# Kernel tuning notes

Measured on AMD Instinct MI355X. Metric: run time of the kernel, lower is better.

The kernel has to match this reference:

```python
import jax, jax.numpy as jnp
import numpy as np

C_M = 256
C_Z = 128
L = 1024


def setup_inputs() -> dict:
    key = jax.random.key(0)
    ks = jax.random.split(key, 8)
    sequence = jax.random.randint(ks[0], (L,), 0, 21)
    residue_index = jnp.arange(L, dtype=jnp.int64) if jax.config.jax_enable_x64 else jnp.arange(L, dtype=jnp.int32)
    # Linear params (torch Linear: y = x @ W.T + b); store as [in, out] for einsum
    W_msa = jax.random.normal(ks[1], (21, C_M), dtype=jnp.float32) * 0.02
    b_msa = jnp.zeros((C_M,), dtype=jnp.float32)
    W_left = jax.random.normal(ks[2], (21, C_Z), dtype=jnp.float32) * 0.02
    b_left = jnp.zeros((C_Z,), dtype=jnp.float32)
    W_right = jax.random.normal(ks[3], (21, C_Z), dtype=jnp.float32) * 0.02
    b_right = jnp.zeros((C_Z,), dtype=jnp.float32)
    relpos_emb = jax.random.normal(ks[4], (65, C_Z), dtype=jnp.float32) * 0.02
    return {
        "sequence": sequence,
        "residue_index": residue_index,
        "W_msa": W_msa, "b_msa": b_msa,
        "W_left": W_left, "b_left": b_left,
        "W_right": W_right, "b_right": b_right,
        "relpos_emb": relpos_emb,
    }


def reference(sequence, residue_index, W_msa, b_msa, W_left, b_left, W_right, b_right, relpos_emb):
    seq = jnp.clip(sequence, 0, 20)
    # one-hot + Linear == row gather of W plus bias; use one_hot matmul to match math exactly
    one_hot = jax.nn.one_hot(seq, 21, dtype=W_msa.dtype)  # [L, 21]
    msa = (one_hot @ W_msa + b_msa)[None]                  # [1, L, c_m]
    left = one_hot @ W_left + b_left                       # [L, c_z]
    right = one_hot @ W_right + b_right                    # [L, c_z]
    d = jnp.clip(residue_index[:, None] - residue_index[None, :] + 32, 0, 64)  # [L, L]
    pair = left[:, None, :] + right[None, :, :] + relpos_emb[d]                # [L, L, c_z]
    return msa, pair
```

## Files before the change

### kernel.cpp

```cpp
#include <hip/hip_runtime.h>

#define L_SEQ 1024
#define CM    256
#define CZ    128
#define NAA   21
#define CHUNK 512
#define NGRP  (CHUNK / 8)

__global__ __launch_bounds__(256, 4) void InputEmbedding_kernel(
    const int*   __restrict__ seq,
    const int*   __restrict__ ri,
    const float* __restrict__ Wm,  const float* __restrict__ bm,
    const float* __restrict__ Wl,  const float* __restrict__ bl,
    const float* __restrict__ Wr,  const float* __restrict__ br,
    const float* __restrict__ rel,
    float* __restrict__ out_msa,
    float* __restrict__ out_pair)
{
    __shared__ float comb   [NAA * CZ];
    __shared__ float comb_lo[NAA * CZ];
    __shared__ float comb_hi[NAA * CZ];
    __shared__ unsigned int sd[CHUNK];

    const int tid = threadIdx.x;
    const int bx  = blockIdx.x;
    const int i   = bx >> 1;
    const int j0  = (bx & 1) * CHUNK;

    int s_i = seq[i];
    s_i = s_i < 0 ? 0 : (s_i > 20 ? 20 : s_i);
    const int rii = ri[i];

    for (int jj = tid; jj < CHUNK; jj += 256) {
        const int j = j0 + jj;
        int sj = seq[j];
        sj = sj < 0 ? 0 : (sj > 20 ? 20 : sj);
        int d = rii - ri[j] + 32;
        d = d < 0 ? 0 : (d > 64 ? 64 : d);
        sd[jj] = (unsigned)(sj * 512) | ((unsigned)(d * 512) << 16);
    }
    for (int idx = tid; idx < NAA * CZ; idx += 256) {
        const int c = idx & (CZ - 1);
        const float cmb = (Wl[s_i * CZ + c] + bl[c]) + (Wr[idx] + br[c]);
        comb[idx]    = cmb;
        comb_lo[idx] = cmb + rel[c];
        comb_hi[idx] = cmb + rel[64 * CZ + c];
    }
    __syncthreads();

    if ((bx & 1) == 0)
        out_msa[i * CM + tid] = Wm[s_i * CM + tid] + bm[tid];

    const int cb = (tid & 31) * 16;
    const int jo = tid >> 5;
    const char* rel_b     = (const char*)rel;
    const char* comb_b    = (const char*)comb;
    const char* comb_lo_b = (const char*)comb_lo;
    const char* comb_hi_b = (const char*)comb_hi;

    const int lo_thresh = i + 32;
    const int hi_thresh = i - 32 - 7;

    float* outp = out_pair + ((size_t)i * L_SEQ + j0 + jo) * CZ + (cb >> 2);

    #pragma unroll 4
    for (int it = 0; it < NGRP; ++it) {
        const int jg = j0 + it * 8;
        const unsigned int p   = sd[it * 8 + jo];
        const unsigned int row = p & 0xFFFFu;

        const bool is_lo  = (jg >= lo_thresh);
        const bool is_hi  = (jg <= hi_thresh);
        const bool is_mid = !(is_lo || is_hi);

        const char* base = is_lo ? comb_lo_b : (is_hi ? comb_hi_b : comb_b);
        float4 v = *(const float4*)(base + row + cb);

        if (is_mid) {
            const float4 rv = *(const float4*)(rel_b + (p >> 16) + cb);
            v.x += rv.x; v.y += rv.y; v.z += rv.z; v.w += rv.w;
        }
        *(float4*)outp = v;
        outp += 8 * CZ;
    }
}

extern "C" void kernel_launch(void* const* d_in, const int* in_sizes, int n_in,
                              void* d_out, int out_size, void* d_ws, size_t ws_size,
                              hipStream_t stream) {
    const int*   seq = (const int*)d_in[0];
    const int*   ri  = (const int*)d_in[1];
    const float* Wm  = (const float*)d_in[2];
    const float* bm  = (const float*)d_in[3];
    const float* Wl  = (const float*)d_in[4];
    const float* bl  = (const float*)d_in[5];
    const float* Wr  = (const float*)d_in[6];
    const float* br  = (const float*)d_in[7];
    const float* rel = (const float*)d_in[8];

    float* out      = (float*)d_out;
    float* out_msa  = out;
    float* out_pair = out + (size_t)L_SEQ * CM;

    hipLaunchKernelGGL(InputEmbedding_kernel, dim3(L_SEQ * 2), dim3(256), 0, stream,
                       seq, ri, Wm, bm, Wl, bl, Wr, br, rel, out_msa, out_pair);
}
```

Baseline: 103.5 us.

## Bucket pair columns by (aa, clipped-distance) class and write from hoisted registers

Adds a per-block counting sort of the column indices into buckets keyed by amino acid and whether the relative distance clips to 0 or 64, using shared-memory atomics and a wave prefix scan. Each bucket's output row is loaded once into registers and scattered to all its columns, and only the unclipped middle band still does a gather plus add. The aim is to cut per-element shared-memory loads and branching in the store loop. In exchange it adds extra barriers, atomics and a scan before any output is written, and the stores become scattered by column order, which may hurt coalescing for a kernel that is bound by writes.

```diff
diff --git a/kernel.cpp b/kernel.cpp
--- a/kernel.cpp
+++ b/kernel.cpp
@@ -5,7 +5,7 @@
 #define CZ    128
 #define NAA   21
 #define CHUNK 512
-#define NGRP  (CHUNK / 8)
+#define NBUCK 42
 
 __global__ __launch_bounds__(256, 4) void InputEmbedding_kernel(
     const int*   __restrict__ seq,
@@ -17,10 +17,13 @@
     float* __restrict__ out_msa,
     float* __restrict__ out_pair)
 {
-    __shared__ float comb   [NAA * CZ];
-    __shared__ float comb_lo[NAA * CZ];
-    __shared__ float comb_hi[NAA * CZ];
-    __shared__ unsigned int sd[CHUNK];
+    __shared__ float comb[NAA * CZ];
+    __shared__ float tbl [NBUCK * CZ];
+    __shared__ unsigned int   sd[CHUNK];
+    __shared__ unsigned short jlist[CHUNK];
+    __shared__ int bcnt[NBUCK + 1];
+    __shared__ int boff[NBUCK + 1];
+    __shared__ int bpos[NBUCK + 1];
 
     const int tid = threadIdx.x;
     const int bx  = blockIdx.x;
@@ -31,6 +34,9 @@
     s_i = s_i < 0 ? 0 : (s_i > 20 ? 20 : s_i);
     const int rii = ri[i];
 
+    if (tid < NBUCK + 1) bcnt[tid] = 0;
+    __syncthreads();
+
     for (int jj = tid; jj < CHUNK; jj += 256) {
         const int j = j0 + jj;
         int sj = seq[j];
@@ -38,50 +44,76 @@
         int d = rii - ri[j] + 32;
         d = d < 0 ? 0 : (d > 64 ? 64 : d);
         sd[jj] = (unsigned)(sj * 512) | ((unsigned)(d * 512) << 16);
+        const int key = (d == 0) ? sj : ((d == 64) ? NAA + sj : NBUCK);
+        atomicAdd(&bcnt[key], 1);
     }
     for (int idx = tid; idx < NAA * CZ; idx += 256) {
         const int c = idx & (CZ - 1);
         const float cmb = (Wl[s_i * CZ + c] + bl[c]) + (Wr[idx] + br[c]);
-        comb[idx]    = cmb;
-        comb_lo[idx] = cmb + rel[c];
-        comb_hi[idx] = cmb + rel[64 * CZ + c];
+        comb[idx]           = cmb;
+        tbl[idx]            = cmb + rel[c];
+        tbl[NAA * CZ + idx] = cmb + rel[64 * CZ + c];
+    }
+    __syncthreads();
+
+    if (tid < 64) {
+        int v = (tid < NBUCK + 1) ? bcnt[tid] : 0;
+        #pragma unroll
+        for (int o = 1; o < 64; o <<= 1) {
+            int u = __shfl_up(v, o, 64);
+            if ((int)tid >= o) v += u;
+        }
+        if (tid < NBUCK + 1) {
+            const int e = v - bcnt[tid];
+            boff[tid] = e;
+            bpos[tid] = e;
+        }
+    }
+    __syncthreads();
+
+    for (int jj = tid; jj < CHUNK; jj += 256) {
+        const unsigned p   = sd[jj];
+        const int d512 = (int)(p >> 16);
+        const int sj   = (int)(p & 0xFFFFu) >> 9;
+        const int key  = (d512 == 0) ? sj : ((d512 == 64 * 512) ? NAA + sj : NBUCK);
+        const int pos  = atomicAdd(&bpos[key], 1);
+        jlist[pos] = (unsigned short)jj;
     }
     __syncthreads();
 
     if ((bx & 1) == 0)
         out_msa[i * CM + tid] = Wm[s_i * CM + tid] + bm[tid];
 
-    const int cb = (tid & 31) * 16;
-    const int jo = tid >> 5;
-    const char* rel_b     = (const char*)rel;
-    const char* comb_b    = (const char*)comb;
-    const char* comb_lo_b = (const char*)comb_lo;
-    const char* comb_hi_b = (const char*)comb_hi;
+    const int wave   = tid >> 6;
+    const int half   = (tid >> 5) & 1;
+    const int cl     = tid & 31;
+    const int kstart = wave * 2 + half;
 
-    const int lo_thresh = i + 32;
-    const int hi_thresh = i - 32 - 7;
+    float* const out_base = out_pair + ((size_t)i * L_SEQ + j0) * CZ + cl * 4;
 
-    float* outp = out_pair + ((size_t)i * L_SEQ + j0 + jo) * CZ + (cb >> 2);
-
-    #pragma unroll 4
-    for (int it = 0; it < NGRP; ++it) {
-        const int jg = j0 + it * 8;
-        const unsigned int p   = sd[it * 8 + jo];
-        const unsigned int row = p & 0xFFFFu;
-
-        const bool is_lo  = (jg >= lo_thresh);
-        const bool is_hi  = (jg <= hi_thresh);
-        const bool is_mid = !(is_lo || is_hi);
-
-        const char* base = is_lo ? comb_lo_b : (is_hi ? comb_hi_b : comb_b);
-        float4 v = *(const float4*)(base + row + cb);
-
-        if (is_mid) {
-            const float4 rv = *(const float4*)(rel_b + (p >> 16) + cb);
-            v.x += rv.x; v.y += rv.y; v.z += rv.z; v.w += rv.w;
+    for (int b = 0; b < NBUCK; ++b) {
+        const int n = bcnt[b];
+        if (n == 0) continue;
+        const int off = boff[b];
+        const float4 v = *reinterpret_cast<const float4*>(&tbl[b * CZ + cl * 4]);
+        for (int k = kstart; k < n; k += 8) {
+            const int jj = jlist[off + k];
+            *reinterpret_cast<float4*>(out_base + (size_t)jj * CZ) = v;
         }
-        *(float4*)outp = v;
-        outp += 8 * CZ;
+    }
+    {
+        const int n   = bcnt[NBUCK];
+        const int off = boff[NBUCK];
+        const char* comb_b = (const char*)comb;
+        const char* rel_b  = (const char*)rel;
+        for (int k = kstart; k < n; k += 8) {
+            const int jj = jlist[off + k];
+            const unsigned p = sd[jj];
+            float4 v = *(const float4*)(comb_b + (p & 0xFFFFu) + cl * 16);
+            const float4 r = *(const float4*)(rel_b + (p >> 16) + cl * 16);
+            v.x += r.x; v.y += r.y; v.z += r.z; v.w += r.w;
+            *reinterpret_cast<float4*>(out_base + (size_t)jj * CZ) = v;
+        }
     }
 }
 
```

New measurement: 107.4 us. 1.04x slower.

## Precompute all 21x21 left+right pair tables in workspace, stream pair output

Applied to the files above, without the earlier changes.

Adds a small prep kernel that writes every (s_i, s_j) combination of left+right, plus copies with the clipped relpos rows added, into the workspace. The main kernel then reads these global tables instead of building three 21x128 shared-memory tables per block. This removes per-block table construction and most of the shared memory, which allows higher occupancy (launch bounds 6). Output writes now use nontemporal stores. The cost is a second launch and reads from the global table that rely on L2 hits, and the old kernel stays as a fallback when the workspace is too small.

```diff
diff --git a/kernel.cpp b/kernel.cpp
--- a/kernel.cpp
+++ b/kernel.cpp
@@ -4,10 +4,93 @@
 #define CM    256
 #define CZ    128
 #define NAA   21
-#define CHUNK 512
-#define NGRP  (CHUNK / 8)
+#define NPAIR (NAA * NAA)
+#define ROWB  (CZ * 4)
+#define TBL_BYTES (3 * NPAIR * ROWB)
 
-__global__ __launch_bounds__(256, 4) void InputEmbedding_kernel(
+typedef float f32x4 __attribute__((ext_vector_type(4)));
+
+static __device__ __forceinline__ int clip21(int s) {
+    return s < 0 ? 0 : (s > 20 ? 20 : s);
+}
+
+__global__ __launch_bounds__(128) void build_tables(
+    const int*   __restrict__ seq,
+    const float* __restrict__ Wl,  const float* __restrict__ bl,
+    const float* __restrict__ Wr,  const float* __restrict__ br,
+    const float* __restrict__ rel,
+    float* __restrict__ ws)
+{
+    const int bx = blockIdx.x;
+    const int si = bx / NAA;
+    const int sj = bx - si * NAA;
+    const int c  = threadIdx.x;
+    (void)seq;
+    const float cmb = (Wl[si * CZ + c] + bl[c]) + (Wr[sj * CZ + c] + br[c]);
+    ws[bx * CZ + c]                 = cmb;
+    ws[NPAIR * CZ + bx * CZ + c]    = cmb + rel[c];
+    ws[2 * NPAIR * CZ + bx * CZ + c] = cmb + rel[64 * CZ + c];
+}
+
+__global__ __launch_bounds__(256, 6) void stream_pair(
+    const int*   __restrict__ seq,
+    const int*   __restrict__ ri,
+    const float* __restrict__ Wm,  const float* __restrict__ bm,
+    const float* __restrict__ rel,
+    const float* __restrict__ ws,
+    float* __restrict__ out_msa,
+    float* __restrict__ out_pair)
+{
+    __shared__ unsigned sd[512];
+    const int tid = threadIdx.x;
+    const int bx  = blockIdx.x;
+    const int i   = bx >> 1;
+    const int j0  = (bx & 1) * 512;
+
+    const int s_i  = clip21(seq[i]);
+    const int rii  = ri[i];
+    const int si21 = s_i * NAA;
+
+    for (int jj = tid; jj < 512; jj += 256) {
+        const int j  = j0 + jj;
+        const int sj = clip21(seq[j]);
+        int d = rii - ri[j] + 32;
+        d = d < 0 ? 0 : (d > 64 ? 64 : d);
+        const unsigned pr = (unsigned)(si21 + sj);
+        sd[jj] = (d == 0)  ? (NPAIR + pr) * ROWB
+               : (d == 64) ? (2u * NPAIR + pr) * ROWB
+               : (0x80000000u | pr | ((unsigned)d << 9));
+    }
+    __syncthreads();
+
+    if ((bx & 1) == 0)
+        out_msa[i * CM + tid] = Wm[s_i * CM + tid] + bm[tid];
+
+    const int cl = tid & 31;
+    const int jo = tid >> 5;
+    const int cb = cl * 16;
+    const char* wsb  = (const char*)ws;
+    const char* relb = (const char*)rel;
+
+    char* outp = (char*)(out_pair + ((size_t)i * L_SEQ + j0 + jo) * CZ) + cb;
+
+    #pragma unroll 8
+    for (int it = 0; it < 64; ++it) {
+        const unsigned p = sd[it * 8 + jo];
+        f32x4 v;
+        if (!(p & 0x80000000u)) {
+            v = *(const f32x4*)(wsb + p + cb);
+        } else {
+            const f32x4 a = *(const f32x4*)(wsb + (p & 0x1FFu) * ROWB + cb);
+            const f32x4 r = *(const f32x4*)(relb + ((p >> 9) & 0x7Fu) * ROWB + cb);
+            v = a + r;
+        }
+        __builtin_nontemporal_store(v, (f32x4*)outp);
+        outp += 8 * ROWB;
+    }
+}
+
+__global__ __launch_bounds__(256, 4) void fallback_kernel(
     const int*   __restrict__ seq,
     const int*   __restrict__ ri,
     const float* __restrict__ Wm,  const float* __restrict__ bm,
@@ -20,21 +103,19 @@
     __shared__ float comb   [NAA * CZ];
     __shared__ float comb_lo[NAA * CZ];
     __shared__ float comb_hi[NAA * CZ];
-    __shared__ unsigned int sd[CHUNK];
+    __shared__ unsigned int sd[512];
 
     const int tid = threadIdx.x;
     const int bx  = blockIdx.x;
     const int i   = bx >> 1;
-    const int j0  = (bx & 1) * CHUNK;
+    const int j0  = (bx & 1) * 512;
 
-    int s_i = seq[i];
-    s_i = s_i < 0 ? 0 : (s_i > 20 ? 20 : s_i);
+    const int s_i = clip21(seq[i]);
     const int rii = ri[i];
 
-    for (int jj = tid; jj < CHUNK; jj += 256) {
+    for (int jj = tid; jj < 512; jj += 256) {
         const int j = j0 + jj;
-        int sj = seq[j];
-        sj = sj < 0 ? 0 : (sj > 20 ? 20 : sj);
+        const int sj = clip21(seq[j]);
         int d = rii - ri[j] + 32;
         d = d < 0 ? 0 : (d > 64 ? 64 : d);
         sd[jj] = (unsigned)(sj * 512) | ((unsigned)(d * 512) << 16);
@@ -57,26 +138,21 @@
     const char* comb_b    = (const char*)comb;
     const char* comb_lo_b = (const char*)comb_lo;
     const char* comb_hi_b = (const char*)comb_hi;
-
     const int lo_thresh = i + 32;
     const int hi_thresh = i - 32 - 7;
 
     float* outp = out_pair + ((size_t)i * L_SEQ + j0 + jo) * CZ + (cb >> 2);
 
     #pragma unroll 4
-    for (int it = 0; it < NGRP; ++it) {
+    for (int it = 0; it < 64; ++it) {
         const int jg = j0 + it * 8;
         const unsigned int p   = sd[it * 8 + jo];
         const unsigned int row = p & 0xFFFFu;
-
-        const bool is_lo  = (jg >= lo_thresh);
-        const bool is_hi  = (jg <= hi_thresh);
-        const bool is_mid = !(is_lo || is_hi);
-
+        const bool is_lo = (jg >= lo_thresh);
+        const bool is_hi = (jg <= hi_thresh);
         const char* base = is_lo ? comb_lo_b : (is_hi ? comb_hi_b : comb_b);
         float4 v = *(const float4*)(base + row + cb);
-
-        if (is_mid) {
+        if (!(is_lo || is_hi)) {
             const float4 rv = *(const float4*)(rel_b + (p >> 16) + cb);
             v.x += rv.x; v.y += rv.y; v.z += rv.z; v.w += rv.w;
         }
@@ -102,6 +178,14 @@
     float* out_msa  = out;
     float* out_pair = out + (size_t)L_SEQ * CM;
 
-    hipLaunchKernelGGL(InputEmbedding_kernel, dim3(L_SEQ * 2), dim3(256), 0, stream,
-                       seq, ri, Wm, bm, Wl, bl, Wr, br, rel, out_msa, out_pair);
+    if (ws_size >= (size_t)TBL_BYTES) {
+        float* ws = (float*)d_ws;
+        hipLaunchKernelGGL(build_tables, dim3(NPAIR), dim3(CZ), 0, stream,
+                           seq, Wl, bl, Wr, br, rel, ws);
+        hipLaunchKernelGGL(stream_pair, dim3(L_SEQ * 2), dim3(256), 0, stream,
+                           seq, ri, Wm, bm, rel, ws, out_msa, out_pair);
+    } else {
+        hipLaunchKernelGGL(fallback_kernel, dim3(L_SEQ * 2), dim3(256), 0, stream,
+                           seq, ri, Wm, bm, Wl, bl, Wr, br, rel, out_msa, out_pair);
+    }
 }
```

After: 112.7 us. 8.9% more time.
